# Performance work log

Measured on AMD Instinct MI355X. Metric: run time of the kernel, lower is better.

The kernel has to match this reference:

```python
import jax, jax.numpy as jnp
import numpy as np

BN_EPS = 1e-5


def setup_inputs() -> dict:
    key = jax.random.key(0)
    ks = jax.random.split(key, 4)
    B, N, D = 8, 8192, 256
    outD = 256
    s = 1.0 / np.sqrt(D)
    return {
        "feature": jax.random.normal(ks[0], (B, N, D), dtype=jnp.float32),
        "W_qk": jax.random.normal(ks[1], (2, D, D), dtype=jnp.float32) * s,
        "b_qk": jnp.zeros((2, D), dtype=jnp.float32),
        "W_v": jax.random.normal(ks[2], (D, outD), dtype=jnp.float32) * s,
        "b_v": jnp.zeros((outD,), dtype=jnp.float32),
        "gamma": jnp.ones((D,), dtype=jnp.float32),
        "beta": jnp.zeros((D,), dtype=jnp.float32),
    }


def reference(feature, W_qk, b_qk, W_v, b_v, gamma, beta):
    # QK: [B, 2, N, D]
    QK = jnp.einsum("bnd,kde->bkne", feature, W_qk) + b_qk[None, :, None, :]
    # value: [B, N, outD]
    value = jnp.einsum("bnd,de->bne", feature, W_v) + b_v
    query = QK[:, 0]  # [B, N, D]
    key = QK[:, 1]    # [B, N, D]
    # softmax over the sequence axis (dim=1), per (batch, channel)
    sm = jax.nn.softmax(key, axis=1)
    # lambda context: softmax^T @ value -> [B, D, outD]
    lam = jnp.einsum("bnd,bne->bde", sm, value)
    # BatchNorm1d(featureDim) in training mode: channel axis = D (axis 1),
    # stats over (batch, spatial) = axes (0, 2); biased variance as torch uses.
    mean = jnp.mean(lam, axis=(0, 2), keepdims=True)
    var = jnp.var(lam, axis=(0, 2), keepdims=True)
    bn = (lam - mean) * jax.lax.rsqrt(var + BN_EPS)
    bn = bn * gamma[None, :, None] + beta[None, :, None]
    # result: query @ BN -> [B, N, outD]
    return jnp.einsum("bnd,bde->bne", query, bn)
```

## Files before the change

### kernel.cpp

```cpp
#include <hip/hip_runtime.h>

typedef unsigned short u16;
typedef __bf16 bf16x8 __attribute__((ext_vector_type(8)));
typedef float f32x4 __attribute__((ext_vector_type(4)));

#define LOG2E 1.44269504088896f

__device__ inline u16 f2b(float f) {
    unsigned u = __float_as_uint(f);
    u += 0x7fff + ((u >> 16) & 1);
    return (u16)(u >> 16);
}
__device__ inline float b2f(u16 u) { return __uint_as_float(((unsigned)u) << 16); }
__device__ inline unsigned pk2(float a, float b) {
    return (unsigned)f2b(a) | ((unsigned)f2b(b) << 16);
}
__device__ inline uint4 pack8(float4 a, float4 b) {
    return uint4{pk2(a.x, a.y), pk2(a.z, a.w), pk2(b.x, b.y), pk2(b.z, b.w)};
}
__device__ inline f32x4 mfma_bf16(uint4 a, uint4 b, f32x4 c) {
    return __builtin_amdgcn_mfma_f32_16x16x32_bf16(
        __builtin_bit_cast(bf16x8, a), __builtin_bit_cast(bf16x8, b), c, 0, 0, 0);
}
__device__ inline void ld16(const u16* g, u16* l) {
    __builtin_amdgcn_global_load_lds(
        (const __attribute__((address_space(1))) unsigned int*)g,
        (__attribute__((address_space(3))) unsigned int*)l, 16, 0, 0);
}
__device__ inline uint4 expfrag(uint4 v, float nc) {
    float e[8];
#pragma unroll
    for (int i = 0; i < 4; ++i) {
        unsigned u = ((const unsigned*)&v)[i];
        e[2 * i] = exp2f(fmaf(b2f((u16)(u & 0xffff)), LOG2E, nc));
        e[2 * i + 1] = exp2f(fmaf(b2f((u16)(u >> 16)), LOG2E, nc));
    }
    uint4 r;
    asm("v_cvt_pk_bf16_f32 %0, %1, %2" : "=v"(r.x) : "v"(e[0]), "v"(e[1]));
    asm("v_cvt_pk_bf16_f32 %0, %1, %2" : "=v"(r.y) : "v"(e[2]), "v"(e[3]));
    asm("v_cvt_pk_bf16_f32 %0, %1, %2" : "=v"(r.z) : "v"(e[4]), "v"(e[5]));
    asm("v_cvt_pk_bf16_f32 %0, %1, %2" : "=v"(r.w) : "v"(e[6]), "v"(e[7]));
    return r;
}


__global__ __launch_bounds__(256) void prep_w(const float* __restrict__ Wqk,
                                              const float* __restrict__ Wv,
                                              u16* __restrict__ WkT,
                                              u16* __restrict__ WvT,
                                              u16* __restrict__ Wqb) {
    int idx = blockIdx.x * 256 + threadIdx.x;
    int which = idx >> 16;
    int i = (idx >> 8) & 255;
    int j = idx & 255;
    if (which == 0)
        WkT[i * 256 + j] = f2b(Wqk[65536 + j * 256 + i]);
    else if (which == 1)
        WvT[i * 256 + j] = f2b(Wv[j * 256 + i]);
    else
        Wqb[i * 256 + j] = f2b(Wqk[i * 256 + j]);
}

__global__ __launch_bounds__(256, 2) void gemm_kv(const float* __restrict__ A,
                                                  const u16* __restrict__ BtK,
                                                  const u16* __restrict__ BtV,
                                                  const float* __restrict__ biasK,
                                                  const float* __restrict__ biasV,
                                                  u16* __restrict__ KT,
                                                  u16* __restrict__ VT,
                                                  float* __restrict__ partial) {
    __shared__ __align__(16) u16 lds[36864];

    const int t = threadIdx.x;
    const int r0 = blockIdx.x * 64;
    const int w = t >> 6, lane = t & 63, l15 = lane & 15, q = lane >> 4;
    const int sq = ((lane & 3) ^ ((lane >> 3) & 3)) * 8;
    const int qs = (q ^ ((l15 >> 1) & 3)) * 8;
    const int awoff = (t >> 2) * 32 + sq;
    const int brr = t >> 2;

    f32x4 accK[4][4], accV[4][4];
#pragma unroll
    for (int rt = 0; rt < 4; ++rt)
#pragma unroll
        for (int ct = 0; ct < 4; ++ct) {
            accK[rt][ct] = f32x4{0.f, 0.f, 0.f, 0.f};
            accV[rt][ct] = f32x4{0.f, 0.f, 0.f, 0.f};
        }

    const float* Arow = A + (long)(r0 + brr) * 256 + (t & 3) * 8;
    float4 p0 = ((const float4*)Arow)[0], p1 = ((const float4*)Arow)[1];
    float4 c0_ = *(const float4*)(Arow + 32), c1_ = *(const float4*)(Arow + 36);
    float4 d0_ = *(const float4*)(Arow + 64), d1_ = *(const float4*)(Arow + 68);

    {
        u16* dK = lds + 4096 + w * 512;
#pragma unroll
        for (int j = 0; j < 4; ++j) {
            int br = j * 64 + brr;
            ld16(BtK + br * 256 + sq, dK + j * 2048);
            ld16(BtV + br * 256 + sq, dK + 8192 + j * 2048);
        }
    }
    *(uint4*)(lds + awoff) = pack8(p0, p1);
    __syncthreads();

#pragma unroll
    for (int t8 = 0; t8 < 8; ++t8) {
        const int cur = t8 & 1;
        if (t8 < 7) {
            const int k0 = (t8 + 1) * 32;
            u16* dK = lds + 4096 + (cur ^ 1) * 16384 + w * 512;
#pragma unroll
            for (int j = 0; j < 4; ++j) {
                int br = j * 64 + brr;
                ld16(BtK + br * 256 + k0 + sq, dK + j * 2048);
                ld16(BtV + br * 256 + k0 + sq, dK + 8192 + j * 2048);
            }
            *(uint4*)(lds + (cur ^ 1) * 2048 + awoff) = pack8(c0_, c1_);
            c0_ = d0_; c1_ = d1_;
            if (t8 < 5) {
                d0_ = *(const float4*)(Arow + (t8 + 3) * 32);
                d1_ = *(const float4*)(Arow + (t8 + 3) * 32 + 4);
            }
        }
        const u16* Asc = lds + cur * 2048;
        const u16* Bc = lds + 4096 + cur * 16384;
        uint4 af[4];
#pragma unroll
        for (int rt = 0; rt < 4; ++rt)
            af[rt] = *(const uint4*)(Asc + (rt * 16 + l15) * 32 + qs);
#pragma unroll
        for (int ct = 0; ct < 4; ++ct) {
            const int bo = (w * 64 + ct * 16 + l15) * 32 + qs;
            uint4 bK = *(const uint4*)(Bc + bo);
            uint4 bV = *(const uint4*)(Bc + 8192 + bo);
#pragma unroll
            for (int rt = 0; rt < 4; ++rt) {
                accK[rt][ct] = mfma_bf16(af[rt], bK, accK[rt][ct]);
                accV[rt][ct] = mfma_bf16(af[rt], bV, accV[rt][ct]);
            }
        }
        __syncthreads();
    }

    const int bb = r0 >> 13;
    const int nt0 = (r0 & 8191) >> 5;
    const int nch = nt0 >> 1;
    u16* Ct = lds;
#pragma unroll
    for (int pass = 0; pass < 2; ++pass) {
        const f32x4(*acc)[4] = pass ? accV : accK;
        const float* bias = pass ? biasV : biasK;
        u16* CT = pass ? VT : KT;
#pragma unroll
        for (int ct = 0; ct < 4; ++ct) {
            const int col = w * 64 + ct * 16 + l15;
            const float bv = bias[col];
            ushort4 pks[4];
#pragma unroll
            for (int rt = 0; rt < 4; ++rt) {
                ushort4 pk;
                pk.x = f2b(acc[rt][ct][0] + bv);
                pk.y = f2b(acc[rt][ct][1] + bv);
                pk.z = f2b(acc[rt][ct][2] + bv);
                pk.w = f2b(acc[rt][ct][3] + bv);
                pks[rt] = pk;
                *(ushort4*)&Ct[col * 72 + rt * 16 + q * 4] = pk;
            }
            if (pass == 0) {
                float zm = -1e30f;
#pragma unroll
                for (int rt = 0; rt < 4; ++rt)
                    zm = fmaxf(zm,
                               fmaxf(fmaxf(b2f(pks[rt].x), b2f(pks[rt].y)),
                                     fmaxf(b2f(pks[rt].z), b2f(pks[rt].w))));
                zm = fmaxf(zm, __shfl_xor(zm, 16, 64));
                zm = fmaxf(zm, __shfl_xor(zm, 32, 64));
                zm *= LOG2E;
                float zs = 0.f;
#pragma unroll
                for (int rt = 0; rt < 4; ++rt) {
                    zs += exp2f(fmaf(b2f(pks[rt].x), LOG2E, -zm));
                    zs += exp2f(fmaf(b2f(pks[rt].y), LOG2E, -zm));
                    zs += exp2f(fmaf(b2f(pks[rt].z), LOG2E, -zm));
                    zs += exp2f(fmaf(b2f(pks[rt].w), LOG2E, -zm));
                }
                zs += __shfl_xor(zs, 16, 64);
                zs += __shfl_xor(zs, 32, 64);
                if (q == 0) {
                    float* pp =
                        partial + (((long)(bb * 128 + nch)) * 256 + col) * 2;
                    pp[0] = zm;
                    pp[1] = zs;
                }
            }
        }
        __syncthreads();
        {
            const long tb = (((long)(bb * 256 + nt0)) * 256 + t) * 32;
#pragma unroll
            for (int j2 = 0; j2 < 2; ++j2)
#pragma unroll
                for (int g = 0; g < 4; ++g)
                    *(uint4*)(CT + tb + j2 * 8192 + g * 8) =
                        *(const uint4*)&Ct[t * 72 + j2 * 32 + g * 8];
        }
        __syncthreads();
    }
}

__global__ __launch_bounds__(256) void stats2(const float* __restrict__ partial,
                                              float* __restrict__ ctab) {
    const int b = blockIdx.x, dg = blockIdx.y;
    const int t = threadIdx.x;
    const int d = dg * 32 + (t & 31);
    const int ci = t >> 5;
    float m = -1e30f, sum = 0.f;
#pragma unroll 4
    for (int k = 0; k < 16; ++k) {
        int i = ci * 16 + k;
        const float* pp = partial + (((long)(b * 128 + i)) * 256 + d) * 2;
        float mi = pp[0], si = pp[1];
        float M = fmaxf(m, mi);
        sum = sum * exp2f(m - M) + si * exp2f(mi - M);
        m = M;
    }
    __shared__ float red[512];
    red[t] = m;
    red[t + 256] = sum;
    __syncthreads();
    if (ci == 0) {
#pragma unroll
        for (int j = 1; j < 8; ++j) {
            float mi = red[t + j * 32], si = red[t + 256 + j * 32];
            float M = fmaxf(m, mi);
            sum = sum * exp2f(m - M) + si * exp2f(mi - M);
            m = M;
        }
        ctab[b * 256 + d] = m + log2f(sum);
    }
}

__global__ __launch_bounds__(256, 3) void gemm_out(const float* __restrict__ A,
                                                   const u16* __restrict__ WfoldT,
                                                   const float* __restrict__ outb,
                                                   float* __restrict__ C) {
    __shared__ __align__(16) u16 lds[20480];
    const int t = threadIdx.x;
    const int r0 = blockIdx.x * 64;
    const int bb = r0 >> 13;
    const int w = t >> 6, lane = t & 63, l15 = lane & 15, q = lane >> 4;
    const int sq = ((lane & 3) ^ ((lane >> 3) & 3)) * 8;
    const int qs = (q ^ ((l15 >> 1) & 3)) * 8;
    const int awoff = (t >> 2) * 32 + sq;
    const int brr = t >> 2;
    const u16* Bt = WfoldT + (long)bb * 65536;

    f32x4 acc[4][4];
#pragma unroll
    for (int rt = 0; rt < 4; ++rt)
#pragma unroll
        for (int ct = 0; ct < 4; ++ct) acc[rt][ct] = f32x4{0.f, 0.f, 0.f, 0.f};

    const float* Arow = A + (long)(r0 + brr) * 256 + (t & 3) * 8;
    float4 p0 = ((const float4*)Arow)[0], p1 = ((const float4*)Arow)[1];
    float4 c0_ = *(const float4*)(Arow + 32), c1_ = *(const float4*)(Arow + 36);
    float4 d0_ = *(const float4*)(Arow + 64), d1_ = *(const float4*)(Arow + 68);

    {
        u16* dB = lds + 4096 + w * 512;
#pragma unroll
        for (int j = 0; j < 4; ++j)
            ld16(Bt + (j * 64 + brr) * 256 + sq, dB + j * 2048);
    }
    *(uint4*)(lds + awoff) = pack8(p0, p1);
    __syncthreads();

#pragma unroll
    for (int t8 = 0; t8 < 8; ++t8) {
        const int cur = t8 & 1;
        if (t8 < 7) {
            const int k0 = (t8 + 1) * 32;
            u16* dB = lds + 4096 + (cur ^ 1) * 8192 + w * 512;
#pragma unroll
            for (int j = 0; j < 4; ++j)
                ld16(Bt + (j * 64 + brr) * 256 + k0 + sq, dB + j * 2048);
            *(uint4*)(lds + (cur ^ 1) * 2048 + awoff) = pack8(c0_, c1_);
            c0_ = d0_; c1_ = d1_;
            if (t8 < 5) {
                d0_ = *(const float4*)(Arow + (t8 + 3) * 32);
                d1_ = *(const float4*)(Arow + (t8 + 3) * 32 + 4);
            }
        }
        const u16* Asc = lds + cur * 2048;
        const u16* Bc = lds + 4096 + cur * 8192;
        uint4 af[4];
#pragma unroll
        for (int rt = 0; rt < 4; ++rt)
            af[rt] = *(const uint4*)(Asc + (rt * 16 + l15) * 32 + qs);
#pragma unroll
        for (int ct = 0; ct < 4; ++ct) {
            uint4 bf = *(const uint4*)(Bc + (w * 64 + ct * 16 + l15) * 32 + qs);
#pragma unroll
            for (int rt = 0; rt < 4; ++rt)
                acc[rt][ct] = mfma_bf16(af[rt], bf, acc[rt][ct]);
        }
        __syncthreads();
    }

#pragma unroll
    for (int ct = 0; ct < 4; ++ct) {
        const int col = w * 64 + ct * 16 + l15;
        const float bv = outb[bb * 256 + col];
#pragma unroll
        for (int rt = 0; rt < 4; ++rt) {
            const long rbase = r0 + rt * 16 + q * 4;
#pragma unroll
            for (int r = 0; r < 4; ++r)
                C[(rbase + r) * 256 + col] = acc[rt][ct][r] + bv;
        }
    }
}

__global__ __launch_bounds__(512, 2) void gemm_lam(const u16* __restrict__ VT,
                                                   const u16* __restrict__ KT,
                                                   const float* __restrict__ ctab,
                                                   float* __restrict__ lamP,
                                                   int nk) {
    __shared__ __align__(16) u16 lds[32768];
    const int t = threadIdx.x;
    const int b = blockIdx.x;
    const int s = blockIdx.y;
    const int w = t >> 6, lane = t & 63, l15 = lane & 15, q = lane >> 4;
    const int eg = w >> 2, dg = w & 3;
    const int sq = ((lane & 3) ^ ((lane >> 3) & 3)) * 8;
    const int qs = (q ^ ((l15 >> 1) & 3)) * 8;

    const int nt0 = s * nk;
    const u16* Vb = VT + ((long)(b * 256 + nt0)) * 8192;
    const u16* Kb = KT + ((long)(b * 256 + nt0)) * 8192;

    float nc[4];
#pragma unroll
    for (int ct = 0; ct < 4; ++ct)
        nc[ct] = -ctab[b * 256 + dg * 64 + ct * 16 + l15];

    f32x4 acc[8][4];
#pragma unroll
    for (int rt = 0; rt < 8; ++rt)
#pragma unroll
        for (int ct = 0; ct < 4; ++ct) acc[rt][ct] = f32x4{0.f, 0.f, 0.f, 0.f};

#define STAGE_TILE(tile, buf)                                                  \
    {                                                                          \
        _Pragma("unroll") for (int j = 0; j < 2; ++j) {                        \
            int g = j * 512 + t;                                               \
            ld16((tile) + (g >> 2) * 32 + sq, (buf) + (j * 512 + w * 64) * 8); \
        }                                                                      \
    }

    STAGE_TILE(Vb, lds)
    STAGE_TILE(Kb, lds + 8192)
    __syncthreads();

    for (int ks = 0; ks < nk; ++ks) {
        const int cur = ks & 1;
        if (ks + 1 < nk) {
            const u16* Vn = Vb + (long)(ks + 1) * 8192;
            const u16* Kn = Kb + (long)(ks + 1) * 8192;
            u16* dst = lds + (cur ^ 1) * 16384;
            STAGE_TILE(Vn, dst)
            STAGE_TILE(Kn, dst + 8192)
        }
        const u16* Vs = lds + cur * 16384;
        const u16* Ks = Vs + 8192;
        uint4 bf[4];
#pragma unroll
        for (int ct = 0; ct < 4; ++ct)
            bf[ct] = expfrag(
                *(const uint4*)(Ks + (dg * 64 + ct * 16 + l15) * 32 + qs),
                nc[ct]);
#pragma unroll
        for (int rt = 0; rt < 8; ++rt) {
            uint4 af = *(const uint4*)(Vs + (eg * 128 + rt * 16 + l15) * 32 + qs);
#pragma unroll
            for (int ct = 0; ct < 4; ++ct)
                acc[rt][ct] = mfma_bf16(af, bf[ct], acc[rt][ct]);
        }
        __syncthreads();
    }
#undef STAGE_TILE

    float* outp = lamP + (long)s * 524288 + (long)b * 65536;
#pragma unroll
    for (int rt = 0; rt < 8; ++rt)
#pragma unroll
        for (int ct = 0; ct < 4; ++ct) {
            const int col = dg * 64 + ct * 16 + l15;
            const int row = eg * 128 + rt * 16 + q * 4;
#pragma unroll
            for (int r = 0; r < 4; ++r)
                outp[(long)(row + r) * 256 + col] = acc[rt][ct][r];
        }
}

__global__ __launch_bounds__(256) void reduce_lam(const float* __restrict__ lamP,
                                                  float* __restrict__ lamT, int S) {
    int i = blockIdx.x * 256 + threadIdx.x;
    float4 v = ((const float4*)lamP)[i];
    for (int s = 1; s < S; ++s) {
        float4 p = ((const float4*)(lamP + (long)s * 524288))[i];
        v.x += p.x; v.y += p.y; v.z += p.z; v.w += p.w;
    }
    ((float4*)lamT)[i] = v;
}

__global__ __launch_bounds__(256, 4) void gemm_fold(const u16* __restrict__ Abn,
                                                    const u16* __restrict__ Wqb,
                                                    u16* __restrict__ WfoldT) {
    __shared__ __align__(16) u16 lds[4096];
    u16* As = lds;
    u16* Bs = lds + 2048;

    const int t = threadIdx.x;
    const int r0 = blockIdx.x * 64;
    const int c0 = blockIdx.y * 64;
    const int w = t >> 6, lane = t & 63, l15 = lane & 15, q = lane >> 4;

    f32x4 acc[4];
#pragma unroll
    for (int c = 0; c < 4; ++c) acc[c] = f32x4{0.f, 0.f, 0.f, 0.f};

    const int br = t >> 2;
    const int bk = (t & 3) * 8;

    for (int k0 = 0; k0 < 256; k0 += 32) {
        ld16(Abn + (long)(r0 + br) * 256 + k0 + bk, As + w * 512);
        ld16(Wqb + (long)(c0 + br) * 256 + k0 + bk, Bs + w * 512);
        __syncthreads();
        uint4 af = *(const uint4*)(As + (w * 16 + l15) * 32 + q * 8);
#pragma unroll
        for (int c = 0; c < 4; ++c) {
            uint4 bf = *(const uint4*)(Bs + (c * 16 + l15) * 32 + q * 8);
            acc[c] = mfma_bf16(af, bf, acc[c]);
        }
        __syncthreads();
    }

#pragma unroll
    for (int c = 0; c < 4; ++c) {
        int col = c0 + c * 16 + l15;
#pragma unroll
        for (int r = 0; r < 4; ++r) {
            int row = r0 + w * 16 + q * 4 + r;
            WfoldT[(long)row * 256 + col] = f2b(acc[c][r]);
        }
    }
}

__global__ __launch_bounds__(256) void bn_kernel(const float* __restrict__ lamT,
                                                 const float* __restrict__ gamma,
                                                 const float* __restrict__ beta,
                                                 u16* __restrict__ bnT) {
    const int d = blockIdx.x;
    const int t = threadIdx.x;
    float vals[8];
    float s = 0.f, ss = 0.f;
#pragma unroll
    for (int i = 0; i < 8; ++i) {
        float v = lamT[(long)(i * 256 + t) * 256 + d];
        vals[i] = v;
        s += v;
        ss += v * v;
    }
#pragma unroll
    for (int sh = 32; sh > 0; sh >>= 1) {
        s += __shfl_xor(s, sh, 64);
        ss += __shfl_xor(ss, sh, 64);
    }
    __shared__ float red[8];
    int w = t >> 6;
    if ((t & 63) == 0) {
        red[w] = s;
        red[w + 4] = ss;
    }
    __syncthreads();
    s = red[0] + red[1] + red[2] + red[3];
    ss = red[4] + red[5] + red[6] + red[7];
    float mean = s * (1.f / 2048.f);
    float var = ss * (1.f / 2048.f) - mean * mean;
    float scale = gamma[d] * rsqrtf(var + 1e-5f);
    float shift = beta[d] - mean * scale;
#pragma unroll
    for (int i = 0; i < 8; ++i)
        bnT[(long)(i * 256 + t) * 256 + d] = f2b(vals[i] * scale + shift);
}

__global__ __launch_bounds__(256) void outb_kernel(const float* __restrict__ bq,
                                                   const u16* __restrict__ bnT,
                                                   float* __restrict__ outb) {
    int b = blockIdx.x, e = threadIdx.x;
    const u16* rowp = bnT + ((long)b * 256 + e) * 256;
    float s = 0.f;
    for (int dd = 0; dd < 256; ++dd) s += bq[dd] * b2f(rowp[dd]);
    outb[b * 256 + e] = s;
}

extern "C" void kernel_launch(void* const* d_in, const int* in_sizes, int n_in,
                              void* d_out, int out_size, void* d_ws, size_t ws_size,
                              hipStream_t stream) {
    const float* feat = (const float*)d_in[0];
    const float* W_qk = (const float*)d_in[1];
    const float* b_qk = (const float*)d_in[2];
    const float* W_v = (const float*)d_in[3];
    const float* b_v = (const float*)d_in[4];
    const float* gamma = (const float*)d_in[5];
    const float* beta = (const float*)d_in[6];
    float* out = (float*)d_out;

    char* ws = (char*)d_ws;
    u16* KT = (u16*)(ws);
    u16* VT = (u16*)(ws + 33554432);
    u16* WkT = (u16*)(ws + 67108864);
    u16* WvT = (u16*)(ws + 67239936);
    u16* Wqb = (u16*)(ws + 67371008);
    float* partial = (float*)(ws + 67502080);
    float* ctab = (float*)(ws + 69599232);
    const size_t base = 69607424;
    float* lamP = (float*)(ws + base);
    size_t avail = (ws_size > base) ? ws_size - base : 0;
    int S = (avail >= 16u * 2097152u) ? 16
          : (avail >= 8u * 2097152u) ? 8
          : (avail >= 4u * 2097152u) ? 4 : 2;
    float* lamT = (float*)ws;
    u16* bnT = (u16*)(ws + 2097152);
    u16* WfoldT = (u16*)(ws + 3145728);
    float* outb = (float*)(ws + 4194304);

    prep_w<<<768, 256, 0, stream>>>(W_qk, W_v, WkT, WvT, Wqb);
    gemm_kv<<<1024, 256, 0, stream>>>(feat, WkT, WvT, b_qk + 256, b_v, KT, VT,
                                      partial);
    stats2<<<dim3(8, 8), 256, 0, stream>>>(partial, ctab);
    gemm_lam<<<dim3(8, S), 512, 0, stream>>>(VT, KT, ctab, lamP, 8192 / S / 32);
    reduce_lam<<<512, 256, 0, stream>>>(lamP, lamT, S);
    bn_kernel<<<256, 256, 0, stream>>>(lamT, gamma, beta, bnT);
    outb_kernel<<<8, 256, 0, stream>>>(b_qk, bnT, outb);
    gemm_fold<<<dim3(32, 4), 256, 0, stream>>>(bnT, Wqb, WfoldT);
    gemm_out<<<1024, 256, 0, stream>>>(feat, WfoldT, outb, out);
}
```

Before: 261.1 us.

## Retile lambda GEMM into smaller blocks, add nontemporal stores, parallelize bias kernel

The lambda GEMM moves from one 512-thread block per batch to eight 256-thread blocks per batch, each owning a 64x128 output tile. This cuts per-block LDS and accumulator use so more blocks fit per CU. The maximum split count S drops from 16 to 8, which reduces partial-sum traffic in reduce_lam. Output and intermediate stores switch to nontemporal stores, and outb_kernel becomes a per-wave dot product with a shuffle reduction across 512 blocks instead of 8 serial blocks. The trade-off is that each block exps the same K tile redundantly across four e-tiles and does less reuse per staged tile.

```diff
diff --git a/kernel.cpp b/kernel.cpp
--- a/kernel.cpp
+++ b/kernel.cpp
@@ -3,6 +3,7 @@
 typedef unsigned short u16;
 typedef __bf16 bf16x8 __attribute__((ext_vector_type(8)));
 typedef float f32x4 __attribute__((ext_vector_type(4)));
+typedef unsigned u32x4 __attribute__((ext_vector_type(4)));
 
 #define LOG2E 1.44269504088896f
 
@@ -26,6 +27,9 @@
     __builtin_amdgcn_global_load_lds(
         (const __attribute__((address_space(1))) unsigned int*)g,
         (__attribute__((address_space(3))) unsigned int*)l, 16, 0, 0);
+}
+__device__ inline void nt_store16(const void* src, void* dst) {
+    __builtin_nontemporal_store(*(const u32x4*)src, (u32x4*)dst);
 }
 __device__ inline uint4 expfrag(uint4 v, float nc) {
     float e[8];
@@ -203,8 +207,8 @@
             for (int j2 = 0; j2 < 2; ++j2)
 #pragma unroll
                 for (int g = 0; g < 4; ++g)
-                    *(uint4*)(CT + tb + j2 * 8192 + g * 8) =
-                        *(const uint4*)&Ct[t * 72 + j2 * 32 + g * 8];
+                    nt_store16(&Ct[t * 72 + j2 * 32 + g * 8],
+                               CT + tb + j2 * 8192 + g * 8);
         }
         __syncthreads();
     }
@@ -318,50 +322,43 @@
             const long rbase = r0 + rt * 16 + q * 4;
 #pragma unroll
             for (int r = 0; r < 4; ++r)
-                C[(rbase + r) * 256 + col] = acc[rt][ct][r] + bv;
-        }
-    }
-}
-
-__global__ __launch_bounds__(512, 2) void gemm_lam(const u16* __restrict__ VT,
+                __builtin_nontemporal_store(acc[rt][ct][r] + bv,
+                                            &C[(rbase + r) * 256 + col]);
+        }
+    }
+}
+
+__global__ __launch_bounds__(256, 6) void gemm_lam(const u16* __restrict__ VT,
                                                    const u16* __restrict__ KT,
                                                    const float* __restrict__ ctab,
                                                    float* __restrict__ lamP,
                                                    int nk) {
-    __shared__ __align__(16) u16 lds[32768];
-    const int t = threadIdx.x;
-    const int b = blockIdx.x;
+    __shared__ __align__(16) u16 lds[12288];
+    const int t = threadIdx.x;
+    const int bx = blockIdx.x;
+    const int b = bx >> 3, e0 = ((bx >> 1) & 3) * 64, d0 = (bx & 1) * 128;
     const int s = blockIdx.y;
     const int w = t >> 6, lane = t & 63, l15 = lane & 15, q = lane >> 4;
-    const int eg = w >> 2, dg = w & 3;
     const int sq = ((lane & 3) ^ ((lane >> 3) & 3)) * 8;
     const int qs = (q ^ ((l15 >> 1) & 3)) * 8;
 
-    const int nt0 = s * nk;
-    const u16* Vb = VT + ((long)(b * 256 + nt0)) * 8192;
-    const u16* Kb = KT + ((long)(b * 256 + nt0)) * 8192;
-
-    float nc[4];
-#pragma unroll
-    for (int ct = 0; ct < 4; ++ct)
-        nc[ct] = -ctab[b * 256 + dg * 64 + ct * 16 + l15];
-
-    f32x4 acc[8][4];
-#pragma unroll
-    for (int rt = 0; rt < 8; ++rt)
-#pragma unroll
-        for (int ct = 0; ct < 4; ++ct) acc[rt][ct] = f32x4{0.f, 0.f, 0.f, 0.f};
-
-#define STAGE_TILE(tile, buf)                                                  \
-    {                                                                          \
-        _Pragma("unroll") for (int j = 0; j < 2; ++j) {                        \
-            int g = j * 512 + t;                                               \
-            ld16((tile) + (g >> 2) * 32 + sq, (buf) + (j * 512 + w * 64) * 8); \
-        }                                                                      \
-    }
-
-    STAGE_TILE(Vb, lds)
-    STAGE_TILE(Kb, lds + 8192)
+    const long nt0 = (long)s * nk;
+    const u16* Vb = VT + ((long)b * 256 + nt0) * 8192;
+    const u16* Kb = KT + ((long)b * 256 + nt0) * 8192;
+
+    float nc0 = -ctab[b * 256 + d0 + w * 32 + l15];
+    float nc1 = -ctab[b * 256 + d0 + w * 32 + 16 + l15];
+
+    f32x4 acc[4][2];
+#pragma unroll
+    for (int rt = 0; rt < 4; ++rt) {
+        acc[rt][0] = f32x4{0.f, 0.f, 0.f, 0.f};
+        acc[rt][1] = f32x4{0.f, 0.f, 0.f, 0.f};
+    }
+
+    ld16(Vb + (e0 + (t >> 2)) * 32 + sq, lds + w * 512);
+    ld16(Kb + (d0 + (t >> 2)) * 32 + sq, lds + 2048 + w * 512);
+    ld16(Kb + (d0 + 64 + (t >> 2)) * 32 + sq, lds + 4096 + w * 512);
     __syncthreads();
 
     for (int ks = 0; ks < nk; ++ks) {
@@ -369,39 +366,36 @@
         if (ks + 1 < nk) {
             const u16* Vn = Vb + (long)(ks + 1) * 8192;
             const u16* Kn = Kb + (long)(ks + 1) * 8192;
-            u16* dst = lds + (cur ^ 1) * 16384;
-            STAGE_TILE(Vn, dst)
-            STAGE_TILE(Kn, dst + 8192)
-        }
-        const u16* Vs = lds + cur * 16384;
-        const u16* Ks = Vs + 8192;
-        uint4 bf[4];
-#pragma unroll
-        for (int ct = 0; ct < 4; ++ct)
-            bf[ct] = expfrag(
-                *(const uint4*)(Ks + (dg * 64 + ct * 16 + l15) * 32 + qs),
-                nc[ct]);
-#pragma unroll
-        for (int rt = 0; rt < 8; ++rt) {
-            uint4 af = *(const uint4*)(Vs + (eg * 128 + rt * 16 + l15) * 32 + qs);
-#pragma unroll
-            for (int ct = 0; ct < 4; ++ct)
-                acc[rt][ct] = mfma_bf16(af, bf[ct], acc[rt][ct]);
-        }
-        __syncthreads();
-    }
-#undef STAGE_TILE
+            u16* dst = lds + (cur ^ 1) * 6144;
+            ld16(Vn + (e0 + (t >> 2)) * 32 + sq, dst + w * 512);
+            ld16(Kn + (d0 + (t >> 2)) * 32 + sq, dst + 2048 + w * 512);
+            ld16(Kn + (d0 + 64 + (t >> 2)) * 32 + sq, dst + 4096 + w * 512);
+        }
+        const u16* Vs = lds + cur * 6144;
+        const u16* Ks = Vs + 2048;
+        uint4 bf0 = expfrag(*(const uint4*)(Ks + (w * 32 + l15) * 32 + qs), nc0);
+        uint4 bf1 =
+            expfrag(*(const uint4*)(Ks + (w * 32 + 16 + l15) * 32 + qs), nc1);
+#pragma unroll
+        for (int rt = 0; rt < 4; ++rt) {
+            uint4 af = *(const uint4*)(Vs + (rt * 16 + l15) * 32 + qs);
+            acc[rt][0] = mfma_bf16(af, bf0, acc[rt][0]);
+            acc[rt][1] = mfma_bf16(af, bf1, acc[rt][1]);
+        }
+        __syncthreads();
+    }
 
     float* outp = lamP + (long)s * 524288 + (long)b * 65536;
 #pragma unroll
-    for (int rt = 0; rt < 8; ++rt)
-#pragma unroll
-        for (int ct = 0; ct < 4; ++ct) {
-            const int col = dg * 64 + ct * 16 + l15;
-            const int row = eg * 128 + rt * 16 + q * 4;
+    for (int rt = 0; rt < 4; ++rt)
+#pragma unroll
+        for (int ct = 0; ct < 2; ++ct) {
+            const int col = d0 + w * 32 + ct * 16 + l15;
+            const int row = e0 + rt * 16 + q * 4;
 #pragma unroll
             for (int r = 0; r < 4; ++r)
-                outp[(long)(row + r) * 256 + col] = acc[rt][ct][r];
+                __builtin_nontemporal_store(
+                    acc[rt][ct][r], &outp[(long)(row + r) * 256 + col]);
         }
 }
 
@@ -500,11 +494,15 @@
 __global__ __launch_bounds__(256) void outb_kernel(const float* __restrict__ bq,
                                                    const u16* __restrict__ bnT,
                                                    float* __restrict__ outb) {
-    int b = blockIdx.x, e = threadIdx.x;
-    const u16* rowp = bnT + ((long)b * 256 + e) * 256;
-    float s = 0.f;
-    for (int dd = 0; dd < 256; ++dd) s += bq[dd] * b2f(rowp[dd]);
-    outb[b * 256 + e] = s;
+    const int t = threadIdx.x;
+    const int wv = t >> 6, lane = t & 63;
+    const int row = blockIdx.x * 4 + wv;
+    ushort4 v = *(const ushort4*)(bnT + (long)row * 256 + lane * 4);
+    float4 g = *(const float4*)(bq + lane * 4);
+    float s = b2f(v.x) * g.x + b2f(v.y) * g.y + b2f(v.z) * g.z + b2f(v.w) * g.w;
+#pragma unroll
+    for (int sh = 32; sh > 0; sh >>= 1) s += __shfl_xor(s, sh, 64);
+    if (lane == 0) outb[row] = s;
 }
 
 extern "C" void kernel_launch(void* const* d_in, const int* in_sizes, int n_in,
@@ -530,8 +528,7 @@
     const size_t base = 69607424;
     float* lamP = (float*)(ws + base);
     size_t avail = (ws_size > base) ? ws_size - base : 0;
-    int S = (avail >= 16u * 2097152u) ? 16
-          : (avail >= 8u * 2097152u) ? 8
+    int S = (avail >= 8u * 2097152u) ? 8
           : (avail >= 4u * 2097152u) ? 4 : 2;
     float* lamT = (float*)ws;
     u16* bnT = (u16*)(ws + 2097152);
@@ -542,10 +539,10 @@
     gemm_kv<<<1024, 256, 0, stream>>>(feat, WkT, WvT, b_qk + 256, b_v, KT, VT,
                                       partial);
     stats2<<<dim3(8, 8), 256, 0, stream>>>(partial, ctab);
-    gemm_lam<<<dim3(8, S), 512, 0, stream>>>(VT, KT, ctab, lamP, 8192 / S / 32);
+    gemm_lam<<<dim3(64, S), 256, 0, stream>>>(VT, KT, ctab, lamP, 8192 / (S * 32));
     reduce_lam<<<512, 256, 0, stream>>>(lamP, lamT, S);
     bn_kernel<<<256, 256, 0, stream>>>(lamT, gamma, beta, bnT);
-    outb_kernel<<<8, 256, 0, stream>>>(b_qk, bnT, outb);
+    outb_kernel<<<512, 256, 0, stream>>>(b_qk, bnT, outb);
     gemm_fold<<<dim3(32, 4), 256, 0, stream>>>(bnT, Wqb, WfoldT);
     gemm_out<<<1024, 256, 0, stream>>>(feat, WfoldT, outb, out);
 }
```

Measured after the change: 305.6 us. 1.17x slower.
